# Kernel tuning notes

Measured on AMD Instinct MI355X. Metric: run time of the kernel, lower is better.

Reference implementation:

```python
import jax, jax.numpy as jnp
import numpy as np

B, S, E, H = 2, 2048, 1024, 16
D = E // H  # head dim = 64
ROPE_BASE = 10000.0


def _rope(x):
    # x: [B, H, S, D]; interleaved-pair rotary embeddings (torchtune style)
    d2 = D // 2
    theta = 1.0 / (ROPE_BASE ** (jnp.arange(d2, dtype=jnp.float32) * 2.0 / D))  # [D/2]
    pos = jnp.arange(S, dtype=jnp.float32)
    ang = pos[:, None] * theta[None, :]            # [S, D/2]
    cos, sin = jnp.cos(ang), jnp.sin(ang)          # broadcast over B,H
    xr = x.reshape(B, H, S, d2, 2)
    x1, x2 = xr[..., 0], xr[..., 1]
    o1 = x1 * cos - x2 * sin
    o2 = x1 * sin + x2 * cos
    return jnp.stack([o1, o2], axis=-1).reshape(B, H, S, D)


def setup_inputs() -> dict:
    key = jax.random.key(0)
    ks = jax.random.split(key, 5)
    scale = 1.0 / np.sqrt(E)
    return {
        "x": jax.random.normal(ks[0], (B, S, E), dtype=jnp.float32),
        "Wq": jax.random.normal(ks[1], (E, E), dtype=jnp.float32) * scale,
        "Wk": jax.random.normal(ks[2], (E, E), dtype=jnp.float32) * scale,
        "Wv": jax.random.normal(ks[3], (E, E), dtype=jnp.float32) * scale,
        "Wo": jax.random.normal(ks[4], (E, E), dtype=jnp.float32) * scale,
    }


def reference(x, Wq, Wk, Wv, Wo):
    # torch Linear: y = x @ W^T
    def proj(W):
        return (x @ W.T).reshape(B, S, H, D).transpose(0, 2, 1, 3)  # [B,H,S,D]

    q = _rope(proj(Wq))
    k = _rope(proj(Wk))
    v = proj(Wv)

    attn_scale = 1.0 / np.sqrt(E)  # faithful: scales by sqrt(d_embed), not head dim
    scores = jnp.einsum('bhqd,bhkd->bhqk', q, k) * attn_scale  # [B,H,S,S]
    causal = jnp.tril(jnp.ones((S, S), dtype=bool))
    scores = jnp.where(causal, scores, -jnp.inf)
    probs = jax.nn.softmax(scores, axis=-1)
    out = jnp.einsum('bhqk,bhkd->bhqd', probs, v)  # [B,H,S,D]
    out = out.transpose(0, 2, 1, 3).reshape(B, S, E)
    return out @ Wo.T
```

## Files before the change

kernel.cpp:

```cpp
#include <hip/hip_runtime.h>
#include <hip/hip_bf16.h>
#include <math.h>

typedef __bf16 bf16;
typedef __bf16 bf16x8 __attribute__((ext_vector_type(8)));
typedef float f32x4 __attribute__((ext_vector_type(4)));

#define SEQ 2048
#define EMB 1024
#define NH  16
#define HD  64
#define NROWS 4096

#define GLOAD_LDS16(gp, lp)                                             \
    __builtin_amdgcn_global_load_lds(                                   \
        (const __attribute__((address_space(1))) void*)(gp),            \
        (__attribute__((address_space(3))) void*)(lp), 16, 0, 0)

__global__ __launch_bounds__(256) void cvt_rope_kernel(
    const float* __restrict__ x,  const float* __restrict__ Wq,
    const float* __restrict__ Wk, const float* __restrict__ Wv,
    const float* __restrict__ Wo,
    bf16* __restrict__ xb, bf16* __restrict__ Wqb, bf16* __restrict__ Wkb,
    bf16* __restrict__ Wvb, bf16* __restrict__ Wob,
    float* __restrict__ ctab, float* __restrict__ stab)
{
    int b = blockIdx.x;
    if (b >= 4096) {
        int t = (b - 4096) * 256 + threadIdx.x;
        int s = t >> 5;
        int j = t & 31;
        double freq = pow(10000.0, -(double)j / 32.0);
        double ang = (double)s * freq;
        ctab[t] = (float)cos(ang);
        stab[t] = (float)sin(ang);
        return;
    }
    const float* src; bf16* dst; int boff;
    if      (b < 2048) { src = x;  dst = xb;  boff = b;        }
    else if (b < 2560) { src = Wq; dst = Wqb; boff = b - 2048; }
    else if (b < 3072) { src = Wk; dst = Wkb; boff = b - 2560; }
    else if (b < 3584) { src = Wv; dst = Wvb; boff = b - 3072; }
    else               { src = Wo; dst = Wob; boff = b - 3584; }
    size_t off = (size_t)boff * 2048 + (size_t)threadIdx.x * 8;
    float4 f0 = *(const float4*)(src + off);
    float4 f1 = *(const float4*)(src + off + 4);
    bf16x8 v;
    v[0] = (bf16)f0.x; v[1] = (bf16)f0.y; v[2] = (bf16)f0.z; v[3] = (bf16)f0.w;
    v[4] = (bf16)f1.x; v[5] = (bf16)f1.y; v[6] = (bf16)f1.z; v[7] = (bf16)f1.w;
    *(bf16x8*)(dst + off) = v;
}

__global__ __launch_bounds__(256) void qkv_rope_kernel(
    const bf16* __restrict__ x,
    const bf16* __restrict__ Wq, const bf16* __restrict__ Wk, const bf16* __restrict__ Wv,
    const float* __restrict__ ctab, const float* __restrict__ stab,
    bf16* __restrict__ q_ws, bf16* __restrict__ kf_ws, bf16* __restrict__ vf_ws)
{
    __shared__ __align__(16) bf16 SMEM[24576];

    const int t    = threadIdx.x;
    const int lane = t & 63;
    const int wave = t >> 6;
    const int col  = lane & 15;
    const int quad = lane >> 4;

    const int nblk = blockIdx.x;
    const int m0   = blockIdx.y * 128;

    const bf16* W; int nloc;
    if (nblk < 8)       { W = Wq; nloc = nblk * 128; }
    else if (nblk < 16) { W = Wk; nloc = (nblk - 8) * 128; }
    else                { W = Wv; nloc = (nblk - 16) * 128; }

    const bf16 *ga[2], *gb[2];
#pragma unroll
    for (int j = 0; j < 2; j++) {
        int c = t + j * 256;
        ga[j] = x + (size_t)(m0 + (c >> 2)) * EMB + (c & 3) * 8;
        gb[j] = W + (size_t)(nloc + (c >> 2)) * EMB + (c & 3) * 8;
    }

    const int wm = (wave >> 1) * 64;
    const int wn = (wave & 1) * 64;

    f32x4 acc[4][4];
#pragma unroll
    for (int i = 0; i < 4; i++)
#pragma unroll
        for (int j = 0; j < 4; j++) acc[i][j] = (f32x4){0.f, 0.f, 0.f, 0.f};

    auto stage = [&](int kt, int b) {
        bf16* As_ = SMEM + b * 8192;
        bf16* Bs_ = As_ + 4096;
        const int kc = kt * 32;
#pragma unroll
        for (int j = 0; j < 2; j++) {
            const int c = t + j * 256;
            GLOAD_LDS16(ga[j] + kc, As_ + c * 8);
            GLOAD_LDS16(gb[j] + kc, Bs_ + c * 8);
        }
    };
    auto compute = [&](int b) {
        bf16* As_ = SMEM + b * 8192;
        bf16* Bs_ = As_ + 4096;
        bf16x8 a[4], bb[4];
#pragma unroll
        for (int mt = 0; mt < 4; mt++)
            a[mt] = *(const bf16x8*)(As_ + (wm + mt * 16 + col) * 32 + quad * 8);
#pragma unroll
        for (int nt = 0; nt < 4; nt++)
            bb[nt] = *(const bf16x8*)(Bs_ + (wn + nt * 16 + col) * 32 + quad * 8);
#pragma unroll
        for (int mt = 0; mt < 4; mt++)
#pragma unroll
            for (int nt = 0; nt < 4; nt++)
                acc[mt][nt] = __builtin_amdgcn_mfma_f32_16x16x32_bf16(a[mt], bb[nt], acc[mt][nt], 0, 0, 0);
    };

    stage(0, 0);
    stage(1, 1);
    int b = 0;
    for (int kt = 0; kt < 31; kt++) {
        asm volatile("s_waitcnt vmcnt(4)\n\ts_barrier" ::: "memory");
        if (kt < 30) stage(kt + 2, (kt + 2) % 3);
        compute(b);
        b = (b == 2) ? 0 : b + 1;
    }
    asm volatile("s_waitcnt vmcnt(0)\n\ts_barrier" ::: "memory");
    compute(b);
    __syncthreads();

    bf16* Es = SMEM + wave * 4608;

    const int n0w  = nblk * 128 + wn;
    const int m0w  = m0 + wm;
    const int bb_  = m0w >> 11;
    const int ss0  = m0w & (SEQ - 1);
    const int h    = (n0w >> 6) & 15;
    const int bh   = bb_ * NH + h;
    const int kind = (n0w < 1024) ? 0 : (n0w < 2048 ? 1 : 2);

#pragma unroll
    for (int mt = 0; mt < 4; mt++) {
#pragma unroll
        for (int nt = 0; nt < 4; nt++) {
            const int d  = nt * 16 + col;
            const int jj = d >> 1;
#pragma unroll
            for (int r = 0; r < 4; r++) {
                const int ss_l = mt * 16 + quad * 4 + r;
                float v = acc[mt][nt][r];
                if (kind < 2) {
                    float partner = __shfl_xor(v, 1, 64);
                    float c  = ctab[(ss0 + ss_l) * 32 + jj];
                    float sn = stab[(ss0 + ss_l) * 32 + jj];
                    float o = ((d & 1) == 0) ? (v * c - partner * sn)
                                             : (partner * sn + v * c);
                    if (kind == 0) {
                        Es[ss_l * 72 + d] = (bf16)(o * 0.03125f);
                    } else {
                        int eoff = ((ss_l >> 4) * 2 + (d >> 5)) * 512
                                 + ((d >> 3) & 3) * 128 + (ss_l & 15) * 8 + (d & 7);
                        Es[eoff] = (bf16)o;
                    }
                } else {
                    int eoff = ((ss_l >> 5) * 4 + (d >> 4)) * 512
                             + ((ss_l >> 3) & 3) * 128 + (d & 15) * 8 + (ss_l & 7);
                    Es[eoff] = (bf16)v;
                }
            }
        }
    }

    const int row = lane >> 3, c8 = lane & 7;
    if (kind == 0) {
        bf16* qbase = q_ws + ((size_t)bh * SEQ + ss0) * HD;
#pragma unroll
        for (int i = 0; i < 8; i++) {
            bf16x8 vv = *(const bf16x8*)&Es[(i * 8 + row) * 72 + c8 * 8];
            *(bf16x8*)(qbase + (size_t)(i * 8 + row) * HD + c8 * 8) = vv;
        }
    } else if (kind == 1) {
        bf16* kbase = kf_ws + ((size_t)bh * 128 + (ss0 >> 4)) * 1024;
#pragma unroll
        for (int i = 0; i < 8; i++) {
            bf16x8 vv = *(const bf16x8*)&Es[i * 512 + lane * 8];
            *(bf16x8*)(kbase + i * 512 + lane * 8) = vv;
        }
    } else {
        bf16* vbase = vf_ws + ((size_t)bh * 64 + (ss0 >> 5)) * 2048;
#pragma unroll
        for (int i = 0; i < 8; i++) {
            bf16x8 vv = *(const bf16x8*)&Es[i * 512 + lane * 8];
            *(bf16x8*)(vbase + i * 512 + lane * 8) = vv;
        }
    }
}

__global__ __launch_bounds__(128) void attn_kernel(
    const bf16* __restrict__ q_ws, const bf16* __restrict__ kf,
    const bf16* __restrict__ vf, bf16* __restrict__ attn_ws)
{
    __shared__ float comb_o[2][4][4][64];
    __shared__ float comb_l[2][64];

    const int lane = threadIdx.x & 63;
    const int wave = threadIdx.x >> 6;
    const int col  = lane & 15;
    const int quad = lane >> 4;

    const int qt = 63 - (int)(blockIdx.x >> 5);
    const int bh = blockIdx.x & 31;
    const int b_ = bh >> 4;
    const int h  = bh & 15;
    const int qb = qt * 32;
    const int nk = qt + 1;

    const bf16* Q  = q_ws + (size_t)bh * SEQ * HD;
    const bf16* Kf = kf + (size_t)bh * 131072;
    const bf16* Vf = vf + (size_t)bh * 131072;

    bf16x8 aq[2][2];
#pragma unroll
    for (int f = 0; f < 2; f++) {
        const bf16* qp = Q + (size_t)(qb + f * 16 + col) * HD + quad * 8;
        aq[f][0] = *(const bf16x8*)(qp);
        aq[f][1] = *(const bf16x8*)(qp + 32);
    }

    f32x4 acc_o[2][4];
#pragma unroll
    for (int f = 0; f < 2; f++)
#pragma unroll
        for (int i = 0; i < 4; i++) acc_o[f][i] = (f32x4){0.f, 0.f, 0.f, 0.f};
    float lsum[2] = {0.f, 0.f};

    int psrc[8];
#pragma unroll
    for (int j = 0; j < 8; j++)
        psrc[j] = ((((quad * 2 + (j >> 2)) & 3) << 4) | col) << 2;

    int s0 = (wave < nk) ? wave : 0;
    bf16x8 Ka[2][2], nKa[2][2];
    {
        const bf16* p = Kf + (size_t)s0 * 2048 + lane * 8;
        Ka[0][0] = *(const bf16x8*)(p);
        Ka[0][1] = *(const bf16x8*)(p + 512);
        Ka[1][0] = *(const bf16x8*)(p + 1024);
        Ka[1][1] = *(const bf16x8*)(p + 1536);
    }

    for (int s = wave; s < nk; s += 2) {
        bf16x8 Vb[4];
        {
            const bf16* p = Vf + (size_t)s * 2048 + lane * 8;
            Vb[0] = *(const bf16x8*)(p);
            Vb[1] = *(const bf16x8*)(p + 512);
            Vb[2] = *(const bf16x8*)(p + 1024);
            Vb[3] = *(const bf16x8*)(p + 1536);
        }

        f32x4 sT[2][2];
#pragma unroll
        for (int g = 0; g < 2; g++)
#pragma unroll
            for (int f = 0; f < 2; f++) {
                f32x4 z = (f32x4){0.f, 0.f, 0.f, 0.f};
                z = __builtin_amdgcn_mfma_f32_16x16x32_bf16(Ka[g][0], aq[f][0], z, 0, 0, 0);
                z = __builtin_amdgcn_mfma_f32_16x16x32_bf16(Ka[g][1], aq[f][1], z, 0, 0, 0);
                sT[g][f] = z;
            }

        {
            int sn = (s + 2 < nk) ? s + 2 : s;
            const bf16* p = Kf + (size_t)sn * 2048 + lane * 8;
            nKa[0][0] = *(const bf16x8*)(p);
            nKa[0][1] = *(const bf16x8*)(p + 512);
            nKa[1][0] = *(const bf16x8*)(p + 1024);
            nKa[1][1] = *(const bf16x8*)(p + 1536);
        }

        float p[2][2][4];
        if (s == nk - 1) {
#pragma unroll
            for (int g = 0; g < 2; g++)
#pragma unroll
                for (int f = 0; f < 2; f++) {
                    const int qg = qb + f * 16 + col;
#pragma unroll
                    for (int r = 0; r < 4; r++) {
                        int key = s * 32 + g * 16 + quad * 4 + r;
                        float e = (key <= qg) ? __expf(sT[g][f][r]) : 0.f;
                        p[g][f][r] = e;
                        lsum[f] += e;
                    }
                }
        } else {
#pragma unroll
            for (int g = 0; g < 2; g++)
#pragma unroll
                for (int f = 0; f < 2; f++)
#pragma unroll
                    for (int r = 0; r < 4; r++) {
                        float e = __expf(sT[g][f][r]);
                        p[g][f][r] = e;
                        lsum[f] += e;
                    }
        }

#pragma unroll
        for (int f = 0; f < 2; f++) {
            unsigned int pk[4];
#pragma unroll
            for (int r = 0; r < 4; r++) {
                unsigned int lo = __builtin_bit_cast(unsigned short, (bf16)p[0][f][r]);
                unsigned int hi = __builtin_bit_cast(unsigned short, (bf16)p[1][f][r]);
                pk[r] = (hi << 16) | lo;
            }
            bf16x8 a_p;
#pragma unroll
            for (int j = 0; j < 8; j++) {
                unsigned int g = (unsigned int)__builtin_amdgcn_ds_bpermute(psrc[j], (int)pk[j & 3]);
                unsigned short bits = (quad < 2) ? (unsigned short)(g & 0xffff)
                                                 : (unsigned short)(g >> 16);
                a_p[j] = __builtin_bit_cast(bf16, bits);
            }
#pragma unroll
            for (int nt = 0; nt < 4; nt++)
                acc_o[f][nt] = __builtin_amdgcn_mfma_f32_16x16x32_bf16(a_p, Vb[nt], acc_o[f][nt], 0, 0, 0);
        }

        Ka[0][0] = nKa[0][0]; Ka[0][1] = nKa[0][1];
        Ka[1][0] = nKa[1][0]; Ka[1][1] = nKa[1][1];
    }

    if (wave == 1) {
#pragma unroll
        for (int f = 0; f < 2; f++) {
            comb_l[f][lane] = lsum[f];
#pragma unroll
            for (int nt = 0; nt < 4; nt++)
#pragma unroll
                for (int r = 0; r < 4; r++)
                    comb_o[f][nt][r][lane] = acc_o[f][nt][r];
        }
    }
    __syncthreads();

    if (wave == 0) {
#pragma unroll
        for (int f = 0; f < 2; f++) {
            lsum[f] += comb_l[f][lane];
#pragma unroll
            for (int nt = 0; nt < 4; nt++)
#pragma unroll
                for (int r = 0; r < 4; r++)
                    acc_o[f][nt][r] += comb_o[f][nt][r][lane];
        }

#pragma unroll
        for (int f = 0; f < 2; f++) {
            lsum[f] += __shfl_xor(lsum[f], 16, 64);
            lsum[f] += __shfl_xor(lsum[f], 32, 64);
        }
#pragma unroll
        for (int f = 0; f < 2; f++)
#pragma unroll
            for (int r = 0; r < 4; r++) {
                float l_r = __shfl(lsum[f], quad * 4 + r, 64);
                float inv = 1.0f / l_r;
                int q = qb + f * 16 + quad * 4 + r;
                bf16* orow = attn_ws + (size_t)(b_ * SEQ + q) * EMB + h * HD;
#pragma unroll
                for (int nt = 0; nt < 4; nt++)
                    orow[nt * 16 + col] = (bf16)(acc_o[f][nt][r] * inv);
            }
    }
}

__global__ __launch_bounds__(256) void oproj_kernel(
    const bf16* __restrict__ attn_ws, const bf16* __restrict__ Wo,
    float* __restrict__ out)
{
    __shared__ __align__(16) char SM[36864];

    const int t    = threadIdx.x;
    const int lane = t & 63;
    const int wave = t >> 6;
    const int col  = lane & 15;
    const int quad = lane >> 4;

    const int n0 = blockIdx.x * 64;
    const int m0 = blockIdx.y * 128;

    const bf16 *ga[2], *gb;
#pragma unroll
    for (int j = 0; j < 2; j++) {
        int c = t + j * 256;
        ga[j] = attn_ws + (size_t)(m0 + (c >> 2)) * EMB + (c & 3) * 8;
    }
    gb = Wo + (size_t)(n0 + (t >> 2)) * EMB + (t & 3) * 8;

    const int wm = (wave >> 1) * 64;
    const int wn = (wave & 1) * 32;

    f32x4 acc[4][2];
#pragma unroll
    for (int i = 0; i < 4; i++)
#pragma unroll
        for (int j = 0; j < 2; j++) acc[i][j] = (f32x4){0.f, 0.f, 0.f, 0.f};

    auto stage = [&](int kt, int b) {
        bf16* As_ = (bf16*)(SM + b * 12288);
        bf16* Bs_ = (bf16*)(SM + b * 12288 + 8192);
        const int kc = kt * 32;
#pragma unroll
        for (int j = 0; j < 2; j++) {
            const int c = t + j * 256;
            GLOAD_LDS16(ga[j] + kc, As_ + c * 8);
        }
        GLOAD_LDS16(gb + kc, Bs_ + t * 8);
    };
    auto compute = [&](int b) {
        bf16* As_ = (bf16*)(SM + b * 12288);
        bf16* Bs_ = (bf16*)(SM + b * 12288 + 8192);
        bf16x8 a[4], bb[2];
#pragma unroll
        for (int mt = 0; mt < 4; mt++)
            a[mt] = *(const bf16x8*)(As_ + (wm + mt * 16 + col) * 32 + quad * 8);
#pragma unroll
        for (int nt = 0; nt < 2; nt++)
            bb[nt] = *(const bf16x8*)(Bs_ + (wn + nt * 16 + col) * 32 + quad * 8);
#pragma unroll
        for (int mt = 0; mt < 4; mt++)
#pragma unroll
            for (int nt = 0; nt < 2; nt++)
                acc[mt][nt] = __builtin_amdgcn_mfma_f32_16x16x32_bf16(a[mt], bb[nt], acc[mt][nt], 0, 0, 0);
    };

    stage(0, 0);
    stage(1, 1);
    int b = 0;
    for (int kt = 0; kt < 31; kt++) {
        asm volatile("s_waitcnt vmcnt(3)\n\ts_barrier" ::: "memory");
        if (kt < 30) stage(kt + 2, (kt + 2) % 3);
        compute(b);
        b = (b == 2) ? 0 : b + 1;
    }
    asm volatile("s_waitcnt vmcnt(0)\n\ts_barrier" ::: "memory");
    compute(b);
    __syncthreads();

    float* Os = (float*)(SM + (size_t)wave * 9216);
#pragma unroll
    for (int mt = 0; mt < 4; mt++)
#pragma unroll
        for (int nt = 0; nt < 2; nt++)
#pragma unroll
            for (int r = 0; r < 4; r++)
                Os[(mt * 16 + quad * 4 + r) * 36 + nt * 16 + col] = acc[mt][nt][r];

    const int row = lane >> 3, c8 = lane & 7;
    float* obase = out + (size_t)(m0 + wm) * EMB + n0 + wn;
#pragma unroll
    for (int i = 0; i < 8; i++) {
        float4 vv = *(const float4*)&Os[(i * 8 + row) * 36 + c8 * 4];
        *(float4*)(obase + (size_t)(i * 8 + row) * EMB + c8 * 4) = vv;
    }
}

extern "C" void kernel_launch(void* const* d_in, const int* in_sizes, int n_in,
                              void* d_out, int out_size, void* d_ws, size_t ws_size,
                              hipStream_t stream) {
    const float* x  = (const float*)d_in[0];
    const float* Wq = (const float*)d_in[1];
    const float* Wk = (const float*)d_in[2];
    const float* Wv = (const float*)d_in[3];
    const float* Wo = (const float*)d_in[4];
    float* out = (float*)d_out;

    char* ws = (char*)d_ws;
    bf16* q_ws    = (bf16*)(ws);
    bf16* kf_ws   = (bf16*)(ws + (8u  << 20));
    bf16* vf_ws   = (bf16*)(ws + (16u << 20));
    bf16* xb      = (bf16*)(ws + (24u << 20));
    bf16* attn_ws = (bf16*)(ws + (24u << 20));
    bf16* Wqb     = (bf16*)(ws + (32u << 20));
    bf16* Wkb     = (bf16*)(ws + (34u << 20));
    bf16* Wvb     = (bf16*)(ws + (36u << 20));
    bf16* Wob     = (bf16*)(ws + (38u << 20));
    float* ctab   = (float*)(ws + (40u << 20));
    float* stab   = ctab + SEQ * 32;

    hipLaunchKernelGGL(cvt_rope_kernel, dim3(4352), dim3(256), 0, stream,
                       x, Wq, Wk, Wv, Wo, xb, Wqb, Wkb, Wvb, Wob, ctab, stab);
    hipLaunchKernelGGL(qkv_rope_kernel, dim3(24, 32), dim3(256), 0, stream,
                       xb, Wqb, Wkb, Wvb, ctab, stab, q_ws, kf_ws, vf_ws);
    hipLaunchKernelGGL(attn_kernel, dim3(2048), dim3(128), 0, stream,
                       q_ws, kf_ws, vf_ws, attn_ws);
    hipLaunchKernelGGL(oproj_kernel, dim3(16, 32), dim3(256), 0, stream,
                       attn_ws, Wob, out);
}
```

Baseline: 175.6 us.

## Enlarge output-projection tile to 128x128 and add MFMA priority hints in attention

The output-projection GEMM tile grows from 128x64 to 128x128, with each wave computing a 64x64 sub-tile. This halves the grid to 256 blocks and raises operand reuse per LDS load, and the epilogue now stages results through LDS in two passes. The attention kernel also wraps its MFMA sections in s_setprio hints so waves doing matrix math are favoured by the scheduler. The trade-off is fewer blocks on a 256-CU part, higher register use for the larger accumulator, and a retuned vmcnt wait count.

```diff
diff --git a/kernel.cpp b/kernel.cpp
--- a/kernel.cpp
+++ b/kernel.cpp
@@ -262,6 +262,7 @@
         }
 
         f32x4 sT[2][2];
+        __builtin_amdgcn_s_setprio(1);
 #pragma unroll
         for (int g = 0; g < 2; g++)
 #pragma unroll
@@ -271,6 +272,7 @@
                 z = __builtin_amdgcn_mfma_f32_16x16x32_bf16(Ka[g][1], aq[f][1], z, 0, 0, 0);
                 sT[g][f] = z;
             }
+        __builtin_amdgcn_s_setprio(0);
 
         {
             int sn = (s + 2 < nk) ? s + 2 : s;
@@ -326,9 +328,11 @@
                                                  : (unsigned short)(g >> 16);
                 a_p[j] = __builtin_bit_cast(bf16, bits);
             }
+            __builtin_amdgcn_s_setprio(1);
 #pragma unroll
             for (int nt = 0; nt < 4; nt++)
                 acc_o[f][nt] = __builtin_amdgcn_mfma_f32_16x16x32_bf16(a_p, Vb[nt], acc_o[f][nt], 0, 0, 0);
+            __builtin_amdgcn_s_setprio(0);
         }
 
         Ka[0][0] = nKa[0][0]; Ka[0][1] = nKa[0][1];
@@ -383,7 +387,7 @@
     const bf16* __restrict__ attn_ws, const bf16* __restrict__ Wo,
     float* __restrict__ out)
 {
-    __shared__ __align__(16) char SM[36864];
+    __shared__ __align__(16) bf16 SMEM[24576];
 
     const int t    = threadIdx.x;
     const int lane = t & 63;
@@ -391,51 +395,51 @@
     const int col  = lane & 15;
     const int quad = lane >> 4;
 
-    const int n0 = blockIdx.x * 64;
+    const int n0 = blockIdx.x * 128;
     const int m0 = blockIdx.y * 128;
 
-    const bf16 *ga[2], *gb;
+    const bf16 *ga[2], *gb[2];
 #pragma unroll
     for (int j = 0; j < 2; j++) {
         int c = t + j * 256;
         ga[j] = attn_ws + (size_t)(m0 + (c >> 2)) * EMB + (c & 3) * 8;
-    }
-    gb = Wo + (size_t)(n0 + (t >> 2)) * EMB + (t & 3) * 8;
+        gb[j] = Wo + (size_t)(n0 + (c >> 2)) * EMB + (c & 3) * 8;
+    }
 
     const int wm = (wave >> 1) * 64;
-    const int wn = (wave & 1) * 32;
-
-    f32x4 acc[4][2];
+    const int wn = (wave & 1) * 64;
+
+    f32x4 acc[4][4];
 #pragma unroll
     for (int i = 0; i < 4; i++)
 #pragma unroll
-        for (int j = 0; j < 2; j++) acc[i][j] = (f32x4){0.f, 0.f, 0.f, 0.f};
+        for (int j = 0; j < 4; j++) acc[i][j] = (f32x4){0.f, 0.f, 0.f, 0.f};
 
     auto stage = [&](int kt, int b) {
-        bf16* As_ = (bf16*)(SM + b * 12288);
-        bf16* Bs_ = (bf16*)(SM + b * 12288 + 8192);
+        bf16* As_ = SMEM + b * 8192;
+        bf16* Bs_ = As_ + 4096;
         const int kc = kt * 32;
 #pragma unroll
         for (int j = 0; j < 2; j++) {
             const int c = t + j * 256;
             GLOAD_LDS16(ga[j] + kc, As_ + c * 8);
-        }
-        GLOAD_LDS16(gb + kc, Bs_ + t * 8);
+            GLOAD_LDS16(gb[j] + kc, Bs_ + c * 8);
+        }
     };
     auto compute = [&](int b) {
-        bf16* As_ = (bf16*)(SM + b * 12288);
-        bf16* Bs_ = (bf16*)(SM + b * 12288 + 8192);
-        bf16x8 a[4], bb[2];
+        bf16* As_ = SMEM + b * 8192;
+        bf16* Bs_ = As_ + 4096;
+        bf16x8 a[4], bb[4];
 #pragma unroll
         for (int mt = 0; mt < 4; mt++)
             a[mt] = *(const bf16x8*)(As_ + (wm + mt * 16 + col) * 32 + quad * 8);
 #pragma unroll
-        for (int nt = 0; nt < 2; nt++)
+        for (int nt = 0; nt < 4; nt++)
             bb[nt] = *(const bf16x8*)(Bs_ + (wn + nt * 16 + col) * 32 + quad * 8);
 #pragma unroll
         for (int mt = 0; mt < 4; mt++)
 #pragma unroll
-            for (int nt = 0; nt < 2; nt++)
+            for (int nt = 0; nt < 4; nt++)
                 acc[mt][nt] = __builtin_amdgcn_mfma_f32_16x16x32_bf16(a[mt], bb[nt], acc[mt][nt], 0, 0, 0);
     };
 
@@ -443,7 +447,7 @@
     stage(1, 1);
     int b = 0;
     for (int kt = 0; kt < 31; kt++) {
-        asm volatile("s_waitcnt vmcnt(3)\n\ts_barrier" ::: "memory");
+        asm volatile("s_waitcnt vmcnt(4)\n\ts_barrier" ::: "memory");
         if (kt < 30) stage(kt + 2, (kt + 2) % 3);
         compute(b);
         b = (b == 2) ? 0 : b + 1;
@@ -452,21 +456,23 @@
     compute(b);
     __syncthreads();
 
-    float* Os = (float*)(SM + (size_t)wave * 9216);
-#pragma unroll
-    for (int mt = 0; mt < 4; mt++)
-#pragma unroll
-        for (int nt = 0; nt < 2; nt++)
-#pragma unroll
-            for (int r = 0; r < 4; r++)
-                Os[(mt * 16 + quad * 4 + r) * 36 + nt * 16 + col] = acc[mt][nt][r];
-
+    float* Os = (float*)SMEM + (size_t)wave * 2304;
     const int row = lane >> 3, c8 = lane & 7;
     float* obase = out + (size_t)(m0 + wm) * EMB + n0 + wn;
 #pragma unroll
-    for (int i = 0; i < 8; i++) {
-        float4 vv = *(const float4*)&Os[(i * 8 + row) * 36 + c8 * 4];
-        *(float4*)(obase + (size_t)(i * 8 + row) * EMB + c8 * 4) = vv;
+    for (int p = 0; p < 2; p++) {
+#pragma unroll
+        for (int mt = 0; mt < 4; mt++)
+#pragma unroll
+            for (int ntl = 0; ntl < 2; ntl++)
+#pragma unroll
+                for (int r = 0; r < 4; r++)
+                    Os[(mt * 16 + quad * 4 + r) * 36 + ntl * 16 + col] = acc[mt][p * 2 + ntl][r];
+#pragma unroll
+        for (int i = 0; i < 8; i++) {
+            float4 vv = *(const float4*)&Os[(i * 8 + row) * 36 + c8 * 4];
+            *(float4*)(obase + (size_t)(i * 8 + row) * EMB + p * 32 + c8 * 4) = vv;
+        }
     }
 }
 
@@ -499,6 +505,6 @@
                        xb, Wqb, Wkb, Wvb, ctab, stab, q_ws, kf_ws, vf_ws);
     hipLaunchKernelGGL(attn_kernel, dim3(2048), dim3(128), 0, stream,
                        q_ws, kf_ws, vf_ws, attn_ws);
-    hipLaunchKernelGGL(oproj_kernel, dim3(16, 32), dim3(256), 0, stream,
+    hipLaunchKernelGGL(oproj_kernel, dim3(8, 32), dim3(256), 0, stream,
                        attn_ws, Wob, out);
 }
```

Measured after the change: 175.6 us. About the same (-0.0%).
